# Kernel tuning notes

Measured on AMD Instinct MI355X. Metric: run time of the kernel, lower is better.

Reference implementation:

```python
import jax, jax.numpy as jnp
import numpy as np

D = 256; H = 8; L = 4; K = 4; AS = 2; HD = D // H
KK = K * K
LEVEL_SHAPES = [(128, 128), (64, 64), (32, 32), (16, 16)]


def _kernel_indices():
    # kernel_size=4 (even): linspace(-1.5, 1.5, 4); stack [j, i] then / K
    idx = jnp.linspace(-1.5, 1.5, K)
    ii, jj = jnp.meshgrid(idx, idx, indexing='ij')
    return jnp.stack([jj, ii], axis=-1).reshape(-1, 2) / K  # (KK, 2)


def _bilinear(vf, g, Hl, Wl):
    # vf: (b, H, Hl*Wl, HD) per-level value; g: (b, l1, H, KK, 2) in [0,1]
    # grid_sample semantics, align_corners=False, zero padding
    b, l1, h, kk, _ = g.shape
    x = g[..., 0] * Wl - 0.5
    y = g[..., 1] * Hl - 0.5
    x0 = jnp.floor(x)
    y0 = jnp.floor(y)
    acc = None
    for dx, dy in ((0, 0), (1, 0), (0, 1), (1, 1)):
        xi = x0 + dx
        yi = y0 + dy
        w = (1.0 - jnp.abs(x - xi)) * (1.0 - jnp.abs(y - yi))
        valid = (xi >= 0) & (xi < Wl) & (yi >= 0) & (yi < Hl)
        idx = (jnp.clip(yi, 0, Hl - 1) * Wl + jnp.clip(xi, 0, Wl - 1)).astype(jnp.int32)
        idx = idx.transpose(0, 2, 1, 3).reshape(b, h, l1 * kk)
        gth = jnp.take_along_axis(vf, idx[..., None], axis=2)  # (b,H,l1*kk,HD)
        ww = (w * valid).transpose(0, 2, 1, 3).reshape(b, h, l1 * kk)
        c = gth * ww[..., None]
        acc = c if acc is None else acc + c
    return acc.reshape(b, h, l1, kk, HD).transpose(0, 2, 1, 3, 4)  # (b,l1,H,kk,HD)


def setup_inputs() -> dict:
    key = jax.random.key(0)
    ks = jax.random.split(key, 9)
    b, l1 = 4, 1024
    l2 = sum(h * w for h, w in LEVEL_SHAPES)  # 21760
    query = jax.random.normal(ks[0], (b, l1, D), jnp.float32)
    value = jax.random.normal(ks[1], (b, l2, D), jnp.float32)
    centers = jax.random.uniform(ks[2], (b, l1, 2), jnp.float32)
    sizes = jax.random.uniform(ks[3], (b, l1, 2), jnp.float32) * 0.2 + 0.05
    ref_windows = jnp.concatenate([centers, sizes], axis=-1)  # (b,l1,4) cx,cy,w,h
    s = 1.0 / np.sqrt(D)
    Wv = jax.random.normal(ks[4], (D, D), jnp.float32) * s
    bv = jnp.zeros((D,), jnp.float32)
    Wo = jax.random.normal(ks[5], (D, D), jnp.float32) * s
    bo = jnp.zeros((D,), jnp.float32)
    Wbox = jax.random.normal(ks[6], (L * H * 4, D), jnp.float32) * 0.01
    bbox = jax.random.uniform(ks[7], (H * L * 4,), jnp.float32)
    Wattn = jax.random.normal(ks[8], (H * L * AS * AS, D), jnp.float32) * s
    battn = jnp.zeros((H * L * AS * AS,), jnp.float32)
    v_shape = np.array(LEVEL_SHAPES, np.int64)
    starts = np.cumsum([0] + [h * w for h, w in LEVEL_SHAPES[:-1]])
    v_start_index = np.array(starts, np.int64)
    v_mask = jnp.zeros((b, l2), bool)
    return dict(query=query, value=value, ref_windows=ref_windows, Wv=Wv, bv=bv,
                Wo=Wo, bo=bo, Wbox=Wbox, bbox=bbox, Wattn=Wattn, battn=battn,
                v_shape=v_shape, v_start_index=v_start_index, v_mask=v_mask)


def reference(query, value, ref_windows, Wv, bv, Wo, bo, Wbox, bbox, Wattn, battn,
              v_shape, v_start_index, v_mask):
    b, l1, _ = query.shape
    l2 = value.shape[1]
    # value projection + padding mask
    v = value @ Wv.T + bv
    v = jnp.where(v_mask[..., None], 0.0, v).reshape(b, l2, H, HD)
    # where to attend: offset boxes -> sampling grid (normalizer=None branch)
    off = (query @ Wbox.T + bbox).reshape(b, l1, H, L, 4)
    refw = ref_windows[:, :, None, None, :]            # (b,l1,1,1,4)
    refsz = jnp.concatenate([refw[..., 2:4], refw[..., 2:4]], axis=-1)
    boxes = refw + off / 8.0 * refsz                   # (b,l1,H,L,4)
    center = boxes[..., None, :2]
    size = boxes[..., None, 2:]
    grid = center + _kernel_indices() * jax.nn.relu(size)  # (b,l1,H,L,KK,2)
    # attention weights (attn_size grid upsampled to kernel_size by repeat_interleave)
    aw = (query @ Wattn.T + battn).reshape(b, l1, H, L, AS, AS)
    nr = K // AS
    aw = jnp.repeat(jnp.repeat(aw, nr, axis=-1), nr, axis=-2)  # (b,l1,H,L,K,K)
    sw = jax.nn.softmax(aw.reshape(b, l1, H, -1), axis=-1).reshape(b, l1, H, L, KK)
    lw = jax.nn.softmax(aw, axis=3).reshape(b, l1, H, L, KK)
    out = jnp.zeros((b, l1, H, HD), query.dtype)
    mout = jnp.zeros((b, l1, H, HD), query.dtype)
    for li in range(L):
        Hl, Wl = int(v_shape[li, 0]), int(v_shape[li, 1])
        st = int(v_start_index[li])
        vf = v[:, st:st + Hl * Wl].transpose(0, 2, 1, 3)  # (b,H,Hl*Wl,HD)
        samp = _bilinear(vf, grid[:, :, :, li], Hl, Wl)   # (b,l1,H,KK,HD)
        out = out + jnp.einsum('bqhkd,bqhk->bqhd', samp, sw[:, :, :, li])
        mout = mout + jnp.einsum('bqhkd,bqhk->bqhd', samp, lw[:, :, :, li])
    out = out.reshape(b, l1, D) @ Wo.T + bo
    mout = mout.reshape(b, l1, D) @ Wo.T + bo
    return out, mout, aw
```

## Files before the change

kernel.cpp:

```cpp
#include <hip/hip_runtime.h>
#include <hip/hip_bf16.h>
#include <hip/hip_fp16.h>


typedef __attribute__((ext_vector_type(8))) short short8;
typedef __attribute__((ext_vector_type(4))) float f32x4;
typedef __attribute__((ext_vector_type(4))) unsigned int uint4v;

__device__ __forceinline__ unsigned short f2bf(float f) {
    unsigned int u = __float_as_uint(f);
    unsigned int r = u + 0x7FFFu + ((u >> 16) & 1u);
    return (unsigned short)(r >> 16);
}
__device__ __forceinline__ unsigned short f2h(float f) {
    __half h = __float2half_rn(f);
    return *reinterpret_cast<unsigned short*>(&h);
}
__device__ __forceinline__ unsigned int pkbf(float a, float b) {
    __hip_bfloat162 h = __float22bfloat162_rn(float2{a, b});
    return *reinterpret_cast<unsigned int*>(&h);
}
__device__ __forceinline__ short8 pack2(float4 x, float4 y) {
    uint4v u;
    u[0] = pkbf(x.x, x.y); u[1] = pkbf(x.z, x.w);
    u[2] = pkbf(y.x, y.y); u[3] = pkbf(y.z, y.w);
    return __builtin_bit_cast(short8, u);
}
__device__ __forceinline__ void gld_lds16(const float* g, float* l) {
    __builtin_amdgcn_global_load_lds(
        (const __attribute__((address_space(1))) unsigned int*)g,
        (__attribute__((address_space(3))) unsigned int*)l, 16, 0, 0);
}

#define TILE_F 4096

__device__ __forceinline__ void gemm_body_v(
    const float* __restrict__ A, const float* __restrict__ W,
    const float* __restrict__ bias, unsigned short* __restrict__ C,
    int bm, int bn, int vb, int pbase, float* AsF)
{
    const int tid  = threadIdx.x;
    const int lane = tid & 63;
    const int wave = tid >> 6;
    const int wm = (wave & 1) * 64;
    const int wn = (wave >> 1) * 64;
    const int kg = lane >> 4;
    const int lm = lane & 15;

    f32x4 acc[4][4];
#pragma unroll
    for (int i = 0; i < 4; ++i)
#pragma unroll
        for (int j = 0; j < 4; ++j) {
            acc[i][j][0] = 0.f; acc[i][j][1] = 0.f;
            acc[i][j][2] = 0.f; acc[i][j][3] = 0.f;
        }

    const int g = (lane & 7) ^ (lane >> 3);
    const float* Ag = A + (size_t)(bm + 32 * wave + (lane >> 3)) * 256 + 4 * g;
    const int ldsw = (32 * wave) * 32;

    const int p0 = (2 * kg) ^ (lm & 7);
    const int p1 = p0 ^ 1;
    const int abase = (wm + lm) * 8;

    const float* Wrow = W + (size_t)(bn + wn + lm) * 256 + kg * 8;

#define STAGE_A(BUF, K0)                                                      \
    {                                                                         \
        _Pragma("unroll")                                                     \
        for (int j = 0; j < 4; ++j)                                           \
            gld_lds16(Ag + (size_t)j * 8 * 256 + (K0),                        \
                      AsF + (BUF) * TILE_F + ldsw + j * 8 * 32);              \
    }
#define LOAD_W(K0)                                                            \
    {                                                                         \
        _Pragma("unroll")                                                     \
        for (int j = 0; j < 4; ++j) {                                         \
            fw[j][0] = *(const float4*)(Wrow + j * 4096 + (K0));              \
            fw[j][1] = *(const float4*)(Wrow + j * 4096 + (K0) + 4);          \
        }                                                                     \
    }

    float4 fw[4][2];

    STAGE_A(0, 0)
    LOAD_W(0)
    asm volatile("s_waitcnt vmcnt(0)" ::: "memory");
    __builtin_amdgcn_s_barrier();

#pragma unroll 2
    for (int it = 0; it < 8; ++it) {
        const int cur = it & 1;
        const int nxt = cur ^ 1;
        if (it < 7) STAGE_A(nxt, 32 * (it + 1))
        short8 bfr[4];
#pragma unroll
        for (int j = 0; j < 4; ++j) bfr[j] = pack2(fw[j][0], fw[j][1]);
        if (it < 7) LOAD_W(32 * (it + 1))
        const float4* Af4 = (const float4*)(AsF + cur * TILE_F);
        short8 af[4];
#pragma unroll
        for (int i = 0; i < 4; ++i) {
            float4 c0 = Af4[abase + i * 128 + p0];
            float4 c1 = Af4[abase + i * 128 + p1];
            af[i] = pack2(c0, c1);
        }
#pragma unroll
        for (int i = 0; i < 4; ++i)
#pragma unroll
            for (int j = 0; j < 4; ++j)
                acc[i][j] = __builtin_amdgcn_mfma_f32_16x16x32_bf16(
                    af[i], bfr[j], acc[i][j], 0, 0, 0);
        if (it < 7) {
            asm volatile("s_waitcnt vmcnt(0) lgkmcnt(0)" ::: "memory");
            __builtin_amdgcn_s_barrier();
            asm volatile("" ::: "memory");
        }
    }
#undef STAGE_A
#undef LOAD_W

    __syncthreads();
    {
        unsigned short* sv = (unsigned short*)AsF;
#pragma unroll
        for (int j = 0; j < 4; ++j) {
            const int cb = wn + j * 16;
            const int pl = cb >> 5;
            const int ch = (cb & 16) + lm;
            const float bcol = bias[bn + cb + lm];
#pragma unroll
            for (int i = 0; i < 4; ++i) {
#pragma unroll
                for (int r = 0; r < 4; ++r) {
                    const int px = wm + i * 16 + kg * 4 + r;
                    sv[(pl * 128 + px) * 32 + ch] = f2h(acc[i][j][r] + bcol);
                }
            }
        }
    }
    __syncthreads();
    {
        const unsigned short* sv = (const unsigned short*)AsF;
        const int plbase = vb * 8 + (bn >> 5);
#pragma unroll
        for (int q = 0; q < 8; ++q) {
            size_t gbase = ((size_t)(plbase + (q >> 1)) * 21760 + pbase) * 32
                         + (q & 1) * 2048 + tid * 8;
            *(uint4v*)&C[gbase] = *(const uint4v*)&sv[q * 2048 + tid * 8];
        }
    }
}

#define LDA 56

__device__ __forceinline__ void gemm_body_f32(
    const float* __restrict__ A, const float* __restrict__ W,
    const float* __restrict__ bias, float* __restrict__ C,
    int N, int bm, int bn, unsigned short* As, unsigned short* Ws)
{
    const int tid  = threadIdx.x;
    const int lane = tid & 63;
    const int wave = tid >> 6;
    const int wm = (wave & 1) * 64;
    const int wn = (wave >> 1) * 64;
    const int lr = tid >> 1;
    const int lh = (tid & 1) * 16;
    const int kg = lane >> 4;
    const int lm = lane & 15;

    f32x4 acc[4][4];
#pragma unroll
    for (int i = 0; i < 4; ++i)
#pragma unroll
        for (int j = 0; j < 4; ++j) {
            acc[i][j][0] = 0.f; acc[i][j][1] = 0.f;
            acc[i][j][2] = 0.f; acc[i][j][3] = 0.f;
        }

    const float* Ap = A + (size_t)(bm + lr) * 256 + lh;
    const float* Wp = W + (size_t)(bn + lr) * 256 + lh;
    unsigned short* Asp = &As[lr * LDA + lh];
    unsigned short* Wsp = &Ws[lr * LDA + lh];

    for (int k0 = 0; k0 < 256; k0 += 32) {
        float4 a0 = *(const float4*)(Ap + k0);
        float4 a1 = *(const float4*)(Ap + k0 + 4);
        float4 a2 = *(const float4*)(Ap + k0 + 8);
        float4 a3 = *(const float4*)(Ap + k0 + 12);
        float4 w0 = *(const float4*)(Wp + k0);
        float4 w1 = *(const float4*)(Wp + k0 + 4);
        float4 w2 = *(const float4*)(Wp + k0 + 8);
        float4 w3 = *(const float4*)(Wp + k0 + 12);
        __syncthreads();
        *(short8*)(Asp)     = pack2(a0, a1);
        *(short8*)(Asp + 8) = pack2(a2, a3);
        *(short8*)(Wsp)     = pack2(w0, w1);
        *(short8*)(Wsp + 8) = pack2(w2, w3);
        __syncthreads();
        short8 af[4], bfr[4];
#pragma unroll
        for (int i = 0; i < 4; ++i)
            af[i] = *(const short8*)&As[(wm + i * 16 + lm) * LDA + kg * 8];
#pragma unroll
        for (int j = 0; j < 4; ++j)
            bfr[j] = *(const short8*)&Ws[(wn + j * 16 + lm) * LDA + kg * 8];
#pragma unroll
        for (int i = 0; i < 4; ++i)
#pragma unroll
            for (int j = 0; j < 4; ++j)
                acc[i][j] = __builtin_amdgcn_mfma_f32_16x16x32_bf16(
                    af[i], bfr[j], acc[i][j], 0, 0, 0);
    }

#pragma unroll
    for (int j = 0; j < 4; ++j) {
        int col = bn + wn + j * 16 + lm;
        float bcol = bias[col];
#pragma unroll
        for (int i = 0; i < 4; ++i)
#pragma unroll
            for (int r = 0; r < 4; ++r) {
                int row = bm + wm + i * 16 + kg * 4 + r;
                C[(size_t)row * N + col] = acc[i][j][r] + bcol;
            }
    }
}

__device__ __forceinline__ void gemm_body_bf16A(
    const unsigned short* __restrict__ A, const float* __restrict__ W,
    const float* __restrict__ bias, float* __restrict__ C,
    int N, int bm, int bn, unsigned short* As, unsigned short* Ws)
{
    const int tid  = threadIdx.x;
    const int lane = tid & 63;
    const int wave = tid >> 6;
    const int wm = (wave & 1) * 64;
    const int wn = (wave >> 1) * 64;
    const int lr = tid >> 1;
    const int lh = (tid & 1) * 16;
    const int kg = lane >> 4;
    const int lm = lane & 15;

    f32x4 acc[4][4];
#pragma unroll
    for (int i = 0; i < 4; ++i)
#pragma unroll
        for (int j = 0; j < 4; ++j) {
            acc[i][j][0] = 0.f; acc[i][j][1] = 0.f;
            acc[i][j][2] = 0.f; acc[i][j][3] = 0.f;
        }

    const unsigned short* Ap = A + (size_t)(bm + lr) * 256 + lh;
    const float* Wp = W + (size_t)(bn + lr) * 256 + lh;
    unsigned short* Asp = &As[lr * LDA + lh];
    unsigned short* Wsp = &Ws[lr * LDA + lh];

    for (int k0 = 0; k0 < 256; k0 += 32) {
        uint4v a01 = *(const uint4v*)(Ap + k0);
        uint4v a23 = *(const uint4v*)(Ap + k0 + 8);
        float4 w0 = *(const float4*)(Wp + k0);
        float4 w1 = *(const float4*)(Wp + k0 + 4);
        float4 w2 = *(const float4*)(Wp + k0 + 8);
        float4 w3 = *(const float4*)(Wp + k0 + 12);
        __syncthreads();
        *(short8*)(Asp)     = __builtin_bit_cast(short8, a01);
        *(short8*)(Asp + 8) = __builtin_bit_cast(short8, a23);
        *(short8*)(Wsp)     = pack2(w0, w1);
        *(short8*)(Wsp + 8) = pack2(w2, w3);
        __syncthreads();
        short8 af[4], bfr[4];
#pragma unroll
        for (int i = 0; i < 4; ++i)
            af[i] = *(const short8*)&As[(wm + i * 16 + lm) * LDA + kg * 8];
#pragma unroll
        for (int j = 0; j < 4; ++j)
            bfr[j] = *(const short8*)&Ws[(wn + j * 16 + lm) * LDA + kg * 8];
#pragma unroll
        for (int i = 0; i < 4; ++i)
#pragma unroll
            for (int j = 0; j < 4; ++j)
                acc[i][j] = __builtin_amdgcn_mfma_f32_16x16x32_bf16(
                    af[i], bfr[j], acc[i][j], 0, 0, 0);
    }

#pragma unroll
    for (int j = 0; j < 4; ++j) {
        int col = bn + wn + j * 16 + lm;
        float bcol = bias[col];
#pragma unroll
        for (int i = 0; i < 4; ++i)
#pragma unroll
            for (int r = 0; r < 4; ++r) {
                int row = bm + wm + i * 16 + kg * 4 + r;
                C[(size_t)row * N + col] = acc[i][j][r] + bcol;
            }
    }
}

__global__ __launch_bounds__(256) void gemm_vq_kernel(
    const float* __restrict__ value, const float* __restrict__ Wv,
    const float* __restrict__ bv, unsigned short* __restrict__ v,
    const float* __restrict__ query,
    const float* __restrict__ Wbox, const float* __restrict__ bbox, float* __restrict__ off,
    const float* __restrict__ Wattn, const float* __restrict__ battn, float* __restrict__ awr)
{
    __shared__ __align__(16) char smem[32768];
    const int x = blockIdx.x;
    if (x < 1360) {
        const int rb = (x >> 4) * 8 + (x & 7);
        const int s  = (x >> 3) & 1;
        const int vb = rb / 170;
        const int pbase = (rb - vb * 170) * 128;
        gemm_body_v(value, Wv, bv, v, rb * 128, s * 128,
                    vb, pbase, (float*)smem);
    } else {
        const int idx = x - 1360;
        const int bm = (idx & 31) * 128;
        unsigned short* As = (unsigned short*)smem;
        unsigned short* Ws = As + 128 * LDA;
        if (idx < 32) gemm_body_f32(query, Wbox, bbox, off, 128, bm, 0, As, Ws);
        else          gemm_body_f32(query, Wattn, battn, awr, 128, bm, 0, As, Ws);
    }
}

__global__ __launch_bounds__(256) void gemm_o_kernel(
    const unsigned short* __restrict__ A, const float* __restrict__ W,
    const float* __restrict__ bias, float* __restrict__ C)
{
    __shared__ __align__(16) unsigned short As[128 * LDA];
    __shared__ __align__(16) unsigned short Ws[128 * LDA];
    gemm_body_bf16A(A, W, bias, C, 256, blockIdx.x * 128, blockIdx.y * 128, As, Ws);
}

__global__ __launch_bounds__(256) void sample_kernel(
    const unsigned short* __restrict__ v, const float* __restrict__ off,
    const float* __restrict__ awr, const float* __restrict__ refw,
    float* __restrict__ aw_out, unsigned short* __restrict__ accb)
{
    const int x   = blockIdx.x;
    const int cls = x & 7;
    const int b   = cls >> 1;
    const int hg  = cls & 1;
    const int bq  = (b << 10) | (x >> 3);
    const int t   = threadIdx.x;

    __shared__ float ref4[4];
    __shared__ float awl[64];
    __shared__ float bxs[64];
    __shared__ float swl[256];
    __shared__ float lwl[256];
    __shared__ int4  tp[16 * 66];

    if (t < 4)  ref4[t] = refw[bq * 4 + t];
    if (t < 64) awl[t] = awr[(size_t)bq * 128 + hg * 64 + t];
    __syncthreads();

    if (t < 64) {
        float o = off[(size_t)bq * 128 + hg * 64 + t];
        int comp = t & 3;
        float r0 = ref4[0], r1 = ref4[1], r2 = ref4[2], r3 = ref4[3];
        float bx;
        if (comp == 0)      bx = r0 + o * 0.125f * r2;
        else if (comp == 1) bx = r1 + o * 0.125f * r3;
        else if (comp == 2) bx = r2 + o * 0.125f * r2;
        else                bx = r3 + o * 0.125f * r3;
        bxs[t] = bx;

        const int hp = t >> 4, r = t & 15;
        float a = awl[t];
        float m = a;
#pragma unroll
        for (int s = 1; s < 16; s <<= 1) m = fmaxf(m, __shfl_xor(m, s, 16));
        float se = expf(a - m);
#pragma unroll
        for (int s = 1; s < 16; s <<= 1) se += __shfl_xor(se, s, 16);
        const float inv_s = 1.0f / (4.0f * se);

        float* awq = aw_out + (size_t)bq * 512 + (4 * hg + hp) * 64;
#pragma unroll
        for (int j = 0; j < 4; ++j) {
            int eidx = r * 4 + j;
            int l  = eidx >> 4;
            int ky = (eidx >> 2) & 3;
            int kx = eidx & 3;
            int pos = (ky >> 1) * 2 + (kx >> 1);
            float raw = awl[hp * 16 + l * 4 + pos];
            swl[hp * 64 + eidx] = expf(raw - m) * inv_s;
            int base = hp * 16 + pos;
            float m2 = awl[base];
#pragma unroll
            for (int li = 1; li < 4; ++li) m2 = fmaxf(m2, awl[base + li * 4]);
            float s2 = 0.f;
#pragma unroll
            for (int li = 0; li < 4; ++li) s2 += expf(awl[base + li * 4] - m2);
            lwl[hp * 64 + eidx] = expf(raw - m2) / s2;
            awq[eidx] = raw;
        }
    }
    __syncthreads();

    {
        const int STs_[4] = {0, 16384, 20480, 21504};
        int e = t;
        int hp = e >> 6, rem = e & 63, l = rem >> 4, kk = rem & 15;
        const float* bx = &bxs[hp * 16 + l * 4];
        float cx = bx[0], cy = bx[1];
        float bw = fmaxf(bx[2], 0.f), bh = fmaxf(bx[3], 0.f);
        float kx = -0.375f + 0.25f * (float)(kk & 3);
        float ky = -0.375f + 0.25f * (float)(kk >> 2);
        int Wl = 128 >> l;
        float xg = (cx + kx * bw) * (float)Wl - 0.5f;
        float yg = (cy + ky * bh) * (float)Wl - 0.5f;
        float x0f = floorf(xg), y0f = floorf(yg);
        int x0 = (int)x0f, y0 = (int)y0f;
        float fx = xg - x0f, fy = yg - y0f;
        float sww = swl[e], lww = lwl[e];
        int rowbase = (b * 8 + 4 * hg + hp) * 21760 + STs_[l];
        int4* dst = &tp[(hp * 4 + l) * 66 + kk * 4];
#pragma unroll
        for (int tap = 0; tap < 4; ++tap) {
            int dx = tap & 1, dy = tap >> 1;
            int xi = x0 + dx, yi = y0 + dy;
            float w = (dx ? fx : 1.f - fx) * (dy ? fy : 1.f - fy);
            if (xi < 0 || xi >= Wl || yi < 0 || yi >= Wl) w = 0.f;
            int xc = min(max(xi, 0), Wl - 1);
            int yc = min(max(yi, 0), Wl - 1);
            unsigned int uo = f2h(w * sww);
            unsigned int um = f2h(w * lww);
            dst[tap] = int4{(rowbase + yc * Wl + xc) << 3,
                            (int)(uo | (uo << 16)),
                            (int)(um | (um << 16)), 0};
        }
    }
    __syncthreads();

    const int hp   = t >> 6;
    const int lane = t & 63;
    const int l    = (lane >> 4) & 3;
    const int sub  = (lane >> 3) & 1;
    const int cl   = lane & 7;
    const uint2* vp = (const uint2*)v;
    const int4* sp = &tp[(hp * 4 + l) * 66 + sub];

    float a0 = 0.f, a1 = 0.f, a2 = 0.f, a3 = 0.f;
    float m0 = 0.f, m1 = 0.f, m2 = 0.f, m3 = 0.f;
#pragma unroll
    for (int oo = 0; oo < 4; ++oo) {
        __half2 zero2 = __float2half2_rn(0.f);
        __half2 ao0 = zero2, ao1 = zero2, am0 = zero2, am1 = zero2;
#pragma unroll
        for (int i = 0; i < 8; ++i) {
            int4 d = sp[2 * (oo * 8 + i)];
            uint2 pv = vp[(size_t)(d.x + cl)];
            __half2 va = __builtin_bit_cast(__half2, pv.x);
            __half2 vb = __builtin_bit_cast(__half2, pv.y);
            __half2 wo = __builtin_bit_cast(__half2, d.y);
            __half2 wm = __builtin_bit_cast(__half2, d.z);
            ao0 = __hfma2(va, wo, ao0); ao1 = __hfma2(vb, wo, ao1);
            am0 = __hfma2(va, wm, am0); am1 = __hfma2(vb, wm, am1);
        }
        float2 f;
        f = __half22float2(ao0); a0 += f.x; a1 += f.y;
        f = __half22float2(ao1); a2 += f.x; a3 += f.y;
        f = __half22float2(am0); m0 += f.x; m1 += f.y;
        f = __half22float2(am1); m2 += f.x; m3 += f.y;
    }
#pragma unroll
    for (int s = 8; s <= 32; s <<= 1) {
        a0 += __shfl_xor(a0, s); a1 += __shfl_xor(a1, s);
        a2 += __shfl_xor(a2, s); a3 += __shfl_xor(a3, s);
        m0 += __shfl_xor(m0, s); m1 += __shfl_xor(m1, s);
        m2 += __shfl_xor(m2, s); m3 += __shfl_xor(m3, s);
    }
    if (lane < 8) {
        size_t base = (size_t)bq * 256 + (4 * hg + hp) * 32 + cl * 4;
        *(uint2*)&accb[base] = uint2{pkbf(a0, a1), pkbf(a2, a3)};
        *(uint2*)&accb[base + (size_t)4096 * 256] = uint2{pkbf(m0, m1), pkbf(m2, m3)};
    }
}

extern "C" void kernel_launch(void* const* d_in, const int* in_sizes, int n_in,
                              void* d_out, int out_size, void* d_ws, size_t ws_size,
                              hipStream_t stream) {
    const float* query = (const float*)d_in[0];
    const float* value = (const float*)d_in[1];
    const float* refw  = (const float*)d_in[2];
    const float* Wv    = (const float*)d_in[3];
    const float* bv    = (const float*)d_in[4];
    const float* Wo    = (const float*)d_in[5];
    const float* bo    = (const float*)d_in[6];
    const float* Wbox  = (const float*)d_in[7];
    const float* bbox  = (const float*)d_in[8];
    const float* Wattn = (const float*)d_in[9];
    const float* battn = (const float*)d_in[10];

    float* out = (float*)d_out;
    float* aw_out = out + 2 * 1048576;

    unsigned short* v = (unsigned short*)d_ws;
    float* off = (float*)((char*)d_ws + 44564480);
    float* awr = off + 524288;
    unsigned short* accb = (unsigned short*)(awr + 524288);

    gemm_vq_kernel<<<1424, 256, 0, stream>>>(value, Wv, bv, v,
                                             query, Wbox, bbox, off,
                                             Wattn, battn, awr);
    sample_kernel<<<8192, 256, 0, stream>>>(v, off, awr, refw, aw_out, accb);
    gemm_o_kernel<<<dim3(64, 2), 256, 0, stream>>>(accb, Wo, bo, out);
}
```

Baseline: 263.3 us.

## Warp-specialize value projection GEMM into producer and consumer waves

```diff
diff --git a/kernel.cpp b/kernel.cpp
--- a/kernel.cpp
+++ b/kernel.cpp
@@ -34,18 +34,23 @@
 
 #define TILE_F 4096
 
-__device__ __forceinline__ void gemm_body_v(
+__device__ __forceinline__ void gemm_body_v_pc(
     const float* __restrict__ A, const float* __restrict__ W,
     const float* __restrict__ bias, unsigned short* __restrict__ C,
-    int bm, int bn, int vb, int pbase, float* AsF)
+    int bm, int bn, int vb, int pbase, float* AsF, float* WsF)
 {
     const int tid  = threadIdx.x;
     const int lane = tid & 63;
     const int wave = tid >> 6;
+
     const int wm = (wave & 1) * 64;
-    const int wn = (wave >> 1) * 64;
+    const int wn = ((wave >> 1) & 1) * 64;
     const int kg = lane >> 4;
     const int lm = lane & 15;
+    const int p0 = (2 * kg) ^ (lm & 7);
+    const int p1 = p0 ^ 1;
+    const int abase = (wm + lm) * 8;
+    const int bbase = (wn + lm) * 8;
 
     f32x4 acc[4][4];
 #pragma unroll
@@ -56,73 +61,61 @@
             acc[i][j][2] = 0.f; acc[i][j][3] = 0.f;
         }
 
-    const int g = (lane & 7) ^ (lane >> 3);
-    const float* Ag = A + (size_t)(bm + 32 * wave + (lane >> 3)) * 256 + 4 * g;
-    const int ldsw = (32 * wave) * 32;
-
-    const int p0 = (2 * kg) ^ (lm & 7);
-    const int p1 = p0 ^ 1;
-    const int abase = (wm + lm) * 8;
-
-    const float* Wrow = W + (size_t)(bn + wn + lm) * 256 + kg * 8;
-
-#define STAGE_A(BUF, K0)                                                      \
-    {                                                                         \
-        _Pragma("unroll")                                                     \
-        for (int j = 0; j < 4; ++j)                                           \
-            gld_lds16(Ag + (size_t)j * 8 * 256 + (K0),                        \
-                      AsF + (BUF) * TILE_F + ldsw + j * 8 * 32);              \
-    }
-#define LOAD_W(K0)                                                            \
-    {                                                                         \
-        _Pragma("unroll")                                                     \
-        for (int j = 0; j < 4; ++j) {                                         \
-            fw[j][0] = *(const float4*)(Wrow + j * 4096 + (K0));              \
-            fw[j][1] = *(const float4*)(Wrow + j * 4096 + (K0) + 4);          \
-        }                                                                     \
-    }
-
-    float4 fw[4][2];
-
-    STAGE_A(0, 0)
-    LOAD_W(0)
-    asm volatile("s_waitcnt vmcnt(0)" ::: "memory");
-    __builtin_amdgcn_s_barrier();
-
-#pragma unroll 2
-    for (int it = 0; it < 8; ++it) {
-        const int cur = it & 1;
-        const int nxt = cur ^ 1;
-        if (it < 7) STAGE_A(nxt, 32 * (it + 1))
-        short8 bfr[4];
-#pragma unroll
-        for (int j = 0; j < 4; ++j) bfr[j] = pack2(fw[j][0], fw[j][1]);
-        if (it < 7) LOAD_W(32 * (it + 1))
-        const float4* Af4 = (const float4*)(AsF + cur * TILE_F);
-        short8 af[4];
-#pragma unroll
-        for (int i = 0; i < 4; ++i) {
-            float4 c0 = Af4[abase + i * 128 + p0];
-            float4 c1 = Af4[abase + i * 128 + p1];
-            af[i] = pack2(c0, c1);
-        }
-#pragma unroll
-        for (int i = 0; i < 4; ++i)
-#pragma unroll
-            for (int j = 0; j < 4; ++j)
-                acc[i][j] = __builtin_amdgcn_mfma_f32_16x16x32_bf16(
-                    af[i], bfr[j], acc[i][j], 0, 0, 0);
-        if (it < 7) {
-            asm volatile("s_waitcnt vmcnt(0) lgkmcnt(0)" ::: "memory");
-            __builtin_amdgcn_s_barrier();
-            asm volatile("" ::: "memory");
-        }
-    }
-#undef STAGE_A
-#undef LOAD_W
+    if (wave >= 4) {
+        const int pw = wave - 4;
+        const int g = (lane & 7) ^ (lane >> 3);
+        const float* Ag = A + (size_t)(bm + 32 * pw + (lane >> 3)) * 256 + 4 * g;
+        const float* Wg = W + (size_t)(bn + 32 * pw + (lane >> 3)) * 256 + 4 * g;
+        const int ldsw = (32 * pw) * 32;
+
+#define STAGE_P(BUF, K0)                                                      \
+        {                                                                     \
+            _Pragma("unroll")                                                 \
+            for (int j = 0; j < 4; ++j) {                                     \
+                gld_lds16(Ag + (size_t)j * 8 * 256 + (K0),                    \
+                          AsF + (BUF) * TILE_F + ldsw + j * 8 * 32);          \
+                gld_lds16(Wg + (size_t)j * 8 * 256 + (K0),                    \
+                          WsF + (BUF) * TILE_F + ldsw + j * 8 * 32);          \
+            }                                                                 \
+        }
+        STAGE_P(0, 0)
+#pragma unroll
+        for (int t = 0; t < 8; ++t) {
+            __syncthreads();
+            if (t < 7) STAGE_P((t + 1) & 1, 32 * (t + 1))
+        }
+#undef STAGE_P
+    } else {
+#pragma unroll
+        for (int t = 0; t < 8; ++t) {
+            __syncthreads();
+            const int cur = t & 1;
+            const float4* Af4 = (const float4*)(AsF + cur * TILE_F);
+            const float4* Wf4 = (const float4*)(WsF + cur * TILE_F);
+            short8 af[4], bfr[4];
+#pragma unroll
+            for (int i = 0; i < 4; ++i) {
+                float4 c0 = Af4[abase + i * 128 + p0];
+                float4 c1 = Af4[abase + i * 128 + p1];
+                af[i] = pack2(c0, c1);
+            }
+#pragma unroll
+            for (int j = 0; j < 4; ++j) {
+                float4 c0 = Wf4[bbase + j * 128 + p0];
+                float4 c1 = Wf4[bbase + j * 128 + p1];
+                bfr[j] = pack2(c0, c1);
+            }
+#pragma unroll
+            for (int i = 0; i < 4; ++i)
+#pragma unroll
+                for (int j = 0; j < 4; ++j)
+                    acc[i][j] = __builtin_amdgcn_mfma_f32_16x16x32_bf16(
+                        af[i], bfr[j], acc[i][j], 0, 0, 0);
+        }
+    }
 
     __syncthreads();
-    {
+    if (wave < 4) {
         unsigned short* sv = (unsigned short*)AsF;
 #pragma unroll
         for (int j = 0; j < 4; ++j) {
@@ -145,10 +138,9 @@
         const unsigned short* sv = (const unsigned short*)AsF;
         const int plbase = vb * 8 + (bn >> 5);
 #pragma unroll
-        for (int q = 0; q < 8; ++q) {
-            size_t gbase = ((size_t)(plbase + (q >> 1)) * 21760 + pbase) * 32
-                         + (q & 1) * 2048 + tid * 8;
-            *(uint4v*)&C[gbase] = *(const uint4v*)&sv[q * 2048 + tid * 8];
+        for (int q = 0; q < 4; ++q) {
+            size_t gbase = ((size_t)(plbase + q) * 21760 + pbase) * 32 + tid * 8;
+            *(uint4v*)&C[gbase] = *(const uint4v*)&sv[q * 4096 + tid * 8];
         }
     }
 }
@@ -299,23 +291,24 @@
     }
 }
 
-__global__ __launch_bounds__(256) void gemm_vq_kernel(
+__global__ __launch_bounds__(512) void gemm_vq_kernel(
     const float* __restrict__ value, const float* __restrict__ Wv,
     const float* __restrict__ bv, unsigned short* __restrict__ v,
     const float* __restrict__ query,
     const float* __restrict__ Wbox, const float* __restrict__ bbox, float* __restrict__ off,
     const float* __restrict__ Wattn, const float* __restrict__ battn, float* __restrict__ awr)
 {
-    __shared__ __align__(16) char smem[32768];
+    __shared__ __align__(16) char smem[65536];
     const int x = blockIdx.x;
     if (x < 1360) {
         const int rb = (x >> 4) * 8 + (x & 7);
         const int s  = (x >> 3) & 1;
         const int vb = rb / 170;
         const int pbase = (rb - vb * 170) * 128;
-        gemm_body_v(value, Wv, bv, v, rb * 128, s * 128,
-                    vb, pbase, (float*)smem);
+        gemm_body_v_pc(value, Wv, bv, v, rb * 128, s * 128,
+                       vb, pbase, (float*)smem, (float*)(smem + 32768));
     } else {
+        if (threadIdx.x >= 256) return;
         const int idx = x - 1360;
         const int bm = (idx & 31) * 128;
         unsigned short* As = (unsigned short*)smem;
@@ -504,7 +497,7 @@
     float* awr = off + 524288;
     unsigned short* accb = (unsigned short*)(awr + 524288);
 
-    gemm_vq_kernel<<<1424, 256, 0, stream>>>(value, Wv, bv, v,
+    gemm_vq_kernel<<<1424, 512, 0, stream>>>(value, Wv, bv, v,
                                              query, Wbox, bbox, off,
                                              Wattn, battn, awr);
     sample_kernel<<<8192, 256, 0, stream>>>(v, off, awr, refw, aw_out, accb);
```

New measurement: 253.6 us. 1.04x faster.
